# Kernel tuning notes

Hardware: AMD Instinct MI355X
Metric: run time of the kernel (lower is better)

Reference implementation:

```python
import jax, jax.numpy as jnp
import numpy as np

N, E = 50000, 800000
D_IN, D_HID, D_OUT = 128, 64, 32
NEG_SLOPE = 0.2


def _gat_layer(h_in, src, dst, W, a_s, a_d, b):
    # h_in: [N, din], W: [din, dout]
    h = h_in @ W                                   # [N, dout]
    alpha_src = h @ a_s                            # [N]
    alpha_dst = h @ a_d                            # [N]
    e = jax.nn.leaky_relu(alpha_src[src] + alpha_dst[dst], NEG_SLOPE)  # [E']
    # segment softmax over incoming edges of each dst node
    m = jax.ops.segment_max(e, dst, num_segments=N)
    ex = jnp.exp(e - m[dst])
    s = jax.ops.segment_sum(ex, dst, num_segments=N)
    w = ex / s[dst]                                # [E']
    out = jax.ops.segment_sum(h[src] * w[:, None], dst, num_segments=N)
    return out + b


def setup_inputs() -> dict:
    key = jax.random.key(0)
    ks = jax.random.split(key, 16)
    x = jax.random.normal(ks[0], (N, D_IN), dtype=jnp.float32)
    edge_index = jax.random.randint(ks[1], (2, E), 0, N, dtype=jnp.int64)
    dims = [(D_IN, D_HID), (D_HID, D_HID), (D_HID, D_OUT)]
    inp = {"x": x, "edge_index": edge_index}
    for i, (din, dout) in enumerate(dims):
        sc = 1.0 / np.sqrt(din)
        inp[f"W{i}"] = jax.random.normal(ks[2 + 4 * i], (din, dout), dtype=jnp.float32) * sc
        inp[f"as{i}"] = jax.random.normal(ks[3 + 4 * i], (dout,), dtype=jnp.float32) * 0.1
        inp[f"ad{i}"] = jax.random.normal(ks[4 + 4 * i], (dout,), dtype=jnp.float32) * 0.1
        inp[f"b{i}"] = jnp.zeros((dout,), dtype=jnp.float32)
    return inp


def reference(x, edge_index, W0, as0, ad0, b0, W1, as1, ad1, b1, W2, as2, ad2, b2):
    # add self loops (PyG GATConv default)
    loop = jnp.arange(N, dtype=edge_index.dtype)
    src = jnp.concatenate([edge_index[0], loop])
    dst = jnp.concatenate([edge_index[1], loop])
    h = jax.nn.relu(_gat_layer(x, src, dst, W0, as0, ad0, b0))
    h = jax.nn.relu(_gat_layer(h, src, dst, W1, as1, ad1, b1))
    h = jnp.tanh(_gat_layer(h, src, dst, W2, as2, ad2, b2))
    return h
```

## Files before the change

### kernel.cpp

```cpp
#include <hip/hip_runtime.h>
#include <hip/hip_fp16.h>
#include <math.h>

#define N_NODES 50000
#define E_EDGES 800000
#define ETOT    (E_EDGES + N_NODES)

#define BUCK_SHIFT 9
#define BUCK_SZ   (1 << BUCK_SHIFT)
#define NBUCK ((N_NODES + BUCK_SZ - 1) >> BUCK_SHIFT)
#define BS_EPT 16
#define BS_THREADS 256
#define BS_EPB (BS_THREADS * BS_EPT)
#define BS_NBLK ((ETOT + BS_EPB - 1) / BS_EPB)

template<int DIN, int DOUT>
__global__ __launch_bounds__(256)
void gemm_alpha_kernel(const float* __restrict__ X, const float* __restrict__ W,
                       const float* __restrict__ a_s, const float* __restrict__ a_d,
                       __half* __restrict__ H16, float* __restrict__ asrc,
                       float* __restrict__ adst)
{
    constexpr int COLG = DOUT / 4;
    constexpr int ROWG = 256 / COLG;
    constexpr int BM   = ROWG * 4;
    constexpr int K4   = DIN / 4;

    __shared__ float Xl[BM * DIN];
    __shared__ float Wl[DIN * DOUT];

    const int tid = threadIdx.x;
    const int row0b = blockIdx.x * BM;

    constexpr int WV = DIN * DOUT / 4;
    for (int i = tid; i < WV; i += 256)
        ((float4*)Wl)[i] = ((const float4*)W)[i];

    constexpr int XV = BM * K4;
    for (int i = tid; i < XV; i += 256) {
        int r  = i / K4;
        int j  = i % K4;
        int gr = row0b + r;
        float4 v = make_float4(0.f, 0.f, 0.f, 0.f);
        if (gr < N_NODES) v = ((const float4*)X)[gr * K4 + j];
        *(float4*)&Xl[r * DIN + ((j ^ ((r >> 2) & 7)) << 2)] = v;
    }
    __syncthreads();

    const int tx = tid % COLG;
    const int ty = tid / COLG;
    const int r0 = ty * 4;
    const int c0 = tx * 4;
    const int swz = ty & 7;

    float acc[4][4] = {};
    for (int kk = 0; kk < DIN; kk += 4) {
        float a[4][4], w[4][4];
        const int jk = ((kk >> 2) ^ swz) << 2;
#pragma unroll
        for (int i = 0; i < 4; ++i)
            *(float4*)a[i] = *(const float4*)&Xl[(r0 + i) * DIN + jk];
#pragma unroll
        for (int j = 0; j < 4; ++j)
            *(float4*)w[j] = *(const float4*)&Wl[(kk + j) * DOUT + c0];
#pragma unroll
        for (int i = 0; i < 4; ++i)
#pragma unroll
            for (int j = 0; j < 4; ++j)
                acc[i][j] = fmaf(a[i][0], w[0][j],
                            fmaf(a[i][1], w[1][j],
                            fmaf(a[i][2], w[2][j],
                            fmaf(a[i][3], w[3][j], acc[i][j]))));
    }

    float as4[4], ad4[4];
    *(float4*)as4 = *(const float4*)&a_s[c0];
    *(float4*)ad4 = *(const float4*)&a_d[c0];

#pragma unroll
    for (int i = 0; i < 4; ++i) {
        const int gr = row0b + r0 + i;
        float ps = acc[i][0] * as4[0] + acc[i][1] * as4[1] +
                   acc[i][2] * as4[2] + acc[i][3] * as4[3];
        float pd = acc[i][0] * ad4[0] + acc[i][1] * ad4[1] +
                   acc[i][2] * ad4[2] + acc[i][3] * ad4[3];
#pragma unroll
        for (int off = COLG / 2; off >= 1; off >>= 1) {
            ps += __shfl_xor(ps, off, 64);
            pd += __shfl_xor(pd, off, 64);
        }
        if (gr < N_NODES) {
            __half2 p01 = __floats2half2_rn(acc[i][0], acc[i][1]);
            __half2 p23 = __floats2half2_rn(acc[i][2], acc[i][3]);
            uint2 pk;
            pk.x = *(unsigned int*)&p01;
            pk.y = *(unsigned int*)&p23;
            *(uint2*)&H16[gr * DOUT + c0] = pk;
            if (tx == 0) { asrc[gr] = ps; adst[gr] = pd; }
        }
    }
}

__global__ __launch_bounds__(128)
void zero98_kernel(int* __restrict__ bcnt)
{
    int i = threadIdx.x;
    if (i < NBUCK) bcnt[i] = 0;
}

__global__ __launch_bounds__(BS_THREADS)
void hist_kernel(const int* __restrict__ ei, int* __restrict__ bcnt)
{
    __shared__ int lcnt[NBUCK];
    const int t = threadIdx.x;
    for (int i = t; i < NBUCK; i += BS_THREADS) lcnt[i] = 0;
    __syncthreads();
    const int e0 = blockIdx.x * BS_EPB;
#pragma unroll
    for (int k = 0; k < BS_EPT; ++k) {
        const int eid = e0 + k * BS_THREADS + t;
        if (eid < ETOT) {
            int dst = (eid < E_EDGES) ? ei[E_EDGES + eid] : (eid - E_EDGES);
            atomicAdd(&lcnt[dst >> BUCK_SHIFT], 1);
        }
    }
    __syncthreads();
    for (int i = t; i < NBUCK; i += BS_THREADS)
        if (lcnt[i] > 0) atomicAdd(&bcnt[i], lcnt[i]);
}

__global__ __launch_bounds__(128)
void scan98_kernel(const int* __restrict__ bcnt, int* __restrict__ cur,
                   int* __restrict__ cur0)
{
    __shared__ int lds[128];
    const int t = threadIdx.x;
    const int v = (t < NBUCK) ? bcnt[t] : 0;
    lds[t] = v;
    __syncthreads();
    for (int off = 1; off < 128; off <<= 1) {
        int u = (t >= off) ? lds[t - off] : 0;
        __syncthreads();
        lds[t] += u;
        __syncthreads();
    }
    if (t < NBUCK) { cur[t] = lds[t] - v; cur0[t] = lds[t] - v; }
}

__global__ __launch_bounds__(BS_THREADS)
void binscatter_kernel(const int* __restrict__ ei, int* __restrict__ cur,
                       unsigned int* __restrict__ tmp)
{
    __shared__ int lcnt[NBUCK];
    __shared__ int lbase[NBUCK];
    const int t = threadIdx.x;
    for (int i = t; i < NBUCK; i += BS_THREADS) lcnt[i] = 0;
    __syncthreads();

    const int e0 = blockIdx.x * BS_EPB;
    unsigned int pk[BS_EPT];
    int rk[BS_EPT];
    int bk[BS_EPT];
#pragma unroll
    for (int k = 0; k < BS_EPT; ++k) {
        const int eid = e0 + k * BS_THREADS + t;
        bk[k] = -1;
        if (eid < ETOT) {
            int src, dst;
            if (eid < E_EDGES) { src = ei[eid]; dst = ei[E_EDGES + eid]; }
            else               { src = dst = eid - E_EDGES; }
            bk[k] = dst >> BUCK_SHIFT;
            pk[k] = ((unsigned int)dst << 16) | (unsigned int)src;
            rk[k] = atomicAdd(&lcnt[bk[k]], 1);
        }
    }
    __syncthreads();
    for (int i = t; i < NBUCK; i += BS_THREADS)
        if (lcnt[i] > 0) lbase[i] = atomicAdd(&cur[i], lcnt[i]);
    __syncthreads();
#pragma unroll
    for (int k = 0; k < BS_EPT; ++k)
        if (bk[k] >= 0) tmp[lbase[bk[k]] + rk[k]] = pk[k];
}

__global__ __launch_bounds__(BUCK_SZ)
void bucket_sort_kernel(const unsigned int* __restrict__ tmp,
                        const int* __restrict__ cur0,
                        const int* __restrict__ bcnt,
                        unsigned int* __restrict__ csr_pk,
                        int* __restrict__ offs)
{
    __shared__ int lcnt[BUCK_SZ];
    __shared__ int loff[BUCK_SZ];
    __shared__ int lcur[BUCK_SZ];
    const int bk = blockIdx.x;
    const int t  = threadIdx.x;
    const int base = cur0[bk];
    const int cnt  = bcnt[bk];

    lcnt[t] = 0;
    __syncthreads();
    for (int i = t; i < cnt; i += BUCK_SZ)
        atomicAdd(&lcnt[(tmp[base + i] >> 16) & (BUCK_SZ - 1)], 1);
    __syncthreads();

    const int v = lcnt[t];
    loff[t] = v;
    __syncthreads();
    for (int off = 1; off < BUCK_SZ; off <<= 1) {
        int u = (t >= off) ? loff[t - off] : 0;
        __syncthreads();
        loff[t] += u;
        __syncthreads();
    }
    const int excl = loff[t] - v;

    const int g = (bk << BUCK_SHIFT) + t;
    if (g <= N_NODES) offs[g] = base + excl;

    lcur[t] = excl;
    __syncthreads();
    for (int i = t; i < cnt; i += BUCK_SZ) {
        const unsigned int pk = tmp[base + i];
        const int l = (pk >> 16) & (BUCK_SZ - 1);
        const int pos = atomicAdd(&lcur[l], 1);
        csr_pk[base + pos] = pk;
    }
}

__global__ __launch_bounds__(256)
void edge_score_kernel(const unsigned int* __restrict__ csr_pk,
                       const float* __restrict__ asrc,
                       const float* __restrict__ adst,
                       float* __restrict__ pbuf)
{
    int i = blockIdx.x * blockDim.x + threadIdx.x;
    if (i >= ETOT) return;
    const unsigned int pk = csr_pk[i];
    float v = asrc[pk & 0xffffu] + adst[pk >> 16];
    v = (v > 0.f) ? v : 0.2f * v;
    pbuf[i] = __expf(fminf(v, 80.f));
}

template<int DOUT, int ACT>
__global__ __launch_bounds__(256)
void node_agg_kernel(const int* __restrict__ offs,
                     const unsigned int* __restrict__ csr_pk,
                     const float* __restrict__ pbuf,
                     const __half* __restrict__ H16,
                     const float* __restrict__ b,
                     float* __restrict__ out)
{
    constexpr int FL    = DOUT / 4;
    constexpr int SLOTS = 64 / FL;
    const int wv   = threadIdx.x >> 6;
    const int lane = threadIdx.x & 63;
    const int fl   = lane % FL;
    const int slot = lane / FL;
    const int node = blockIdx.x * 4 + wv;
    if (node >= N_NODES) return;

    const int beg = offs[node];
    const int end = offs[node + 1];
    const __half* __restrict__ Hf = H16 + fl * 4;

    float s = 0.f;
    float4 acc = make_float4(0.f, 0.f, 0.f, 0.f);

    for (int cb = beg; cb < end; cb += SLOTS) {
        const int eid = cb + slot;
        float p = 0.f;
        uint2 h8 = make_uint2(0u, 0u);
        if (eid < end) {
            const unsigned int pk = csr_pk[eid];
            p  = pbuf[eid];
            h8 = *(const uint2*)(Hf + (pk & 0xffffu) * DOUT);
        }
        const float2 f01 = __half22float2(*(const __half2*)&h8.x);
        const float2 f23 = __half22float2(*(const __half2*)&h8.y);
        s += p;
        acc.x = fmaf(p, f01.x, acc.x);
        acc.y = fmaf(p, f01.y, acc.y);
        acc.z = fmaf(p, f23.x, acc.z);
        acc.w = fmaf(p, f23.y, acc.w);
    }

#pragma unroll
    for (int off = FL; off < 64; off <<= 1) {
        s     += __shfl_xor(s, off, 64);
        acc.x += __shfl_xor(acc.x, off, 64);
        acc.y += __shfl_xor(acc.y, off, 64);
        acc.z += __shfl_xor(acc.z, off, 64);
        acc.w += __shfl_xor(acc.w, off, 64);
    }

    if (slot == 0) {
        const float4 bb = *(const float4*)&b[fl * 4];
        const float inv = 1.f / s;
        float4 v;
        v.x = acc.x * inv + bb.x;
        v.y = acc.y * inv + bb.y;
        v.z = acc.z * inv + bb.z;
        v.w = acc.w * inv + bb.w;
        if (ACT == 0) {
            v.x = fmaxf(v.x, 0.f); v.y = fmaxf(v.y, 0.f);
            v.z = fmaxf(v.z, 0.f); v.w = fmaxf(v.w, 0.f);
        } else {
            v.x = tanhf(v.x); v.y = tanhf(v.y);
            v.z = tanhf(v.z); v.w = tanhf(v.w);
        }
        *(float4*)&out[node * DOUT + fl * 4] = v;
    }
}


template<int DIN, int DOUT, int ACT>
static void run_layer(const float* X, const float* W, const float* a_s,
                      const float* a_d, const float* b,
                      const int* offs, const unsigned int* csr_pk,
                      float* pbuf, __half* H16, float* asrc, float* adst,
                      float* out, hipStream_t stream)
{
    constexpr int COLG = DOUT / 4;
    constexpr int BM = (256 / COLG) * 4;
    const int gemm_grid = (N_NODES + BM - 1) / BM;
    gemm_alpha_kernel<DIN, DOUT><<<gemm_grid, 256, 0, stream>>>(
        X, W, a_s, a_d, H16, asrc, adst);

    const int egrid = (ETOT + 255) / 256;
    edge_score_kernel<<<egrid, 256, 0, stream>>>(csr_pk, asrc, adst, pbuf);

    const int agg_grid = (N_NODES + 3) / 4;
    node_agg_kernel<DOUT, ACT><<<agg_grid, 256, 0, stream>>>(
        offs, csr_pk, pbuf, H16, b, out);
}

extern "C" void kernel_launch(void* const* d_in, const int* in_sizes, int n_in,
                              void* d_out, int out_size, void* d_ws, size_t ws_size,
                              hipStream_t stream)
{
    const float* x  = (const float*)d_in[0];
    const int*   ei = (const int*)d_in[1];
    const float* W0 = (const float*)d_in[2];
    const float* as0= (const float*)d_in[3];
    const float* ad0= (const float*)d_in[4];
    const float* b0 = (const float*)d_in[5];
    const float* W1 = (const float*)d_in[6];
    const float* as1= (const float*)d_in[7];
    const float* ad1= (const float*)d_in[8];
    const float* b1 = (const float*)d_in[9];
    const float* W2 = (const float*)d_in[10];
    const float* as2= (const float*)d_in[11];
    const float* ad2= (const float*)d_in[12];
    const float* b2 = (const float*)d_in[13];
    float* out = (float*)d_out;

    char* wsb = (char*)d_ws;
    auto take = [&](size_t bytes) {
        char* p = wsb;
        wsb += (bytes + 255) & ~size_t(255);
        return p;
    };
    __half* h16    = (__half*)take(sizeof(__half) * N_NODES * 64);
    float* buf_act = (float*)take(sizeof(float) * N_NODES * 64);
    float* pbuf    = (float*)take(sizeof(float) * ETOT);
    float* asrc    = (float*)take(sizeof(float) * N_NODES);
    float* adst    = (float*)take(sizeof(float) * N_NODES);
    int*   offs    = (int*)take(sizeof(int) * (N_NODES + 1));
    int*   bcnt    = (int*)take(sizeof(int) * NBUCK);
    int*   cur     = (int*)take(sizeof(int) * NBUCK);
    int*   cur0    = (int*)take(sizeof(int) * NBUCK);
    unsigned int* csr_pk = (unsigned int*)take(sizeof(unsigned int) * ETOT);
    unsigned int* tmp = (unsigned int*)h16;

    const int egrid = (ETOT + 255) / 256;
    zero98_kernel<<<1, 128, 0, stream>>>(bcnt);
    hist_kernel<<<BS_NBLK, BS_THREADS, 0, stream>>>(ei, bcnt);
    scan98_kernel<<<1, 128, 0, stream>>>(bcnt, cur, cur0);
    binscatter_kernel<<<BS_NBLK, BS_THREADS, 0, stream>>>(ei, cur, tmp);
    bucket_sort_kernel<<<NBUCK, BUCK_SZ, 0, stream>>>(tmp, cur0, bcnt,
                                                      csr_pk, offs);

    run_layer<128, 64, 0>(x, W0, as0, ad0, b0, offs, csr_pk, pbuf,
                          h16, asrc, adst, buf_act, stream);
    run_layer<64, 64, 0>(buf_act, W1, as1, ad1, b1, offs, csr_pk, pbuf,
                         h16, asrc, adst, buf_act, stream);
    run_layer<64, 32, 1>(buf_act, W2, as2, ad2, b2, offs, csr_pk, pbuf,
                         h16, asrc, adst, out, stream);
}
```

Before: 203.9 us.

## Fuse CSR build into cooperative kernel and inline edge scores into aggregation

Replaces the five CSR-construction launches with a single cooperative kernel that uses grid-wide syncs between the histogram, scan, bin-scatter and bucket-sort phases. The separate edge_score kernel and its pbuf buffer are removed; the aggregation kernel now computes the leaky-relu exponent per edge inline from asrc and the node's adst. Aggregation also moves to 8 features per lane with 16-byte half loads and prefetches the next packed edge. The aim is fewer launches and less edge-sized global traffic. The cost is that the cooperative launch needs all blocks co-resident, and recomputing the exponent inside the gather loop adds work there.

```diff
diff --git a/kernel.cpp b/kernel.cpp
--- a/kernel.cpp
+++ b/kernel.cpp
@@ -1,6 +1,9 @@
 #include <hip/hip_runtime.h>
 #include <hip/hip_fp16.h>
+#include <hip/hip_cooperative_groups.h>
 #include <math.h>
+
+namespace cg = cooperative_groups;
 
 #define N_NODES 50000
 #define E_EDGES 800000
@@ -9,10 +12,10 @@
 #define BUCK_SHIFT 9
 #define BUCK_SZ   (1 << BUCK_SHIFT)
 #define NBUCK ((N_NODES + BUCK_SZ - 1) >> BUCK_SHIFT)
-#define BS_EPT 16
-#define BS_THREADS 256
-#define BS_EPB (BS_THREADS * BS_EPT)
-#define BS_NBLK ((ETOT + BS_EPB - 1) / BS_EPB)
+#define CSR_THREADS 512
+#define CSR_EPT 8
+#define CSR_EPB (CSR_THREADS * CSR_EPT)
+#define CSR_NBLK ((ETOT + CSR_EPB - 1) / CSR_EPB)
 
 template<int DIN, int DOUT>
 __global__ __launch_bounds__(256)
@@ -101,157 +104,126 @@
     }
 }
 
-__global__ __launch_bounds__(128)
-void zero98_kernel(int* __restrict__ bcnt)
-{
-    int i = threadIdx.x;
-    if (i < NBUCK) bcnt[i] = 0;
-}
-
-__global__ __launch_bounds__(BS_THREADS)
-void hist_kernel(const int* __restrict__ ei, int* __restrict__ bcnt)
-{
-    __shared__ int lcnt[NBUCK];
-    const int t = threadIdx.x;
-    for (int i = t; i < NBUCK; i += BS_THREADS) lcnt[i] = 0;
+__global__ __launch_bounds__(CSR_THREADS)
+void csr_build_kernel(const int* __restrict__ ei, int* __restrict__ bpart,
+                      int* __restrict__ cur, int* __restrict__ cur0,
+                      int* __restrict__ bcnt, unsigned int* __restrict__ tmp,
+                      unsigned int* __restrict__ csr_pk, int* __restrict__ offs)
+{
+    cg::grid_group grid = cg::this_grid();
+    __shared__ int lcnt[CSR_THREADS];
+    __shared__ int lextra[CSR_THREADS];
+    const int t   = threadIdx.x;
+    const int blk = blockIdx.x;
+
+    if (t < NBUCK) lcnt[t] = 0;
     __syncthreads();
-    const int e0 = blockIdx.x * BS_EPB;
-#pragma unroll
-    for (int k = 0; k < BS_EPT; ++k) {
-        const int eid = e0 + k * BS_THREADS + t;
-        if (eid < ETOT) {
-            int dst = (eid < E_EDGES) ? ei[E_EDGES + eid] : (eid - E_EDGES);
-            atomicAdd(&lcnt[dst >> BUCK_SHIFT], 1);
+    {
+        const int e0 = blk * CSR_EPB;
+#pragma unroll
+        for (int k = 0; k < CSR_EPT; ++k) {
+            const int eid = e0 + k * CSR_THREADS + t;
+            if (eid < ETOT) {
+                int dst = (eid < E_EDGES) ? ei[E_EDGES + eid] : (eid - E_EDGES);
+                atomicAdd(&lcnt[dst >> BUCK_SHIFT], 1);
+            }
         }
     }
     __syncthreads();
-    for (int i = t; i < NBUCK; i += BS_THREADS)
-        if (lcnt[i] > 0) atomicAdd(&bcnt[i], lcnt[i]);
-}
-
-__global__ __launch_bounds__(128)
-void scan98_kernel(const int* __restrict__ bcnt, int* __restrict__ cur,
-                   int* __restrict__ cur0)
-{
-    __shared__ int lds[128];
-    const int t = threadIdx.x;
-    const int v = (t < NBUCK) ? bcnt[t] : 0;
-    lds[t] = v;
-    __syncthreads();
-    for (int off = 1; off < 128; off <<= 1) {
-        int u = (t >= off) ? lds[t - off] : 0;
-        __syncthreads();
-        lds[t] += u;
-        __syncthreads();
-    }
-    if (t < NBUCK) { cur[t] = lds[t] - v; cur0[t] = lds[t] - v; }
-}
-
-__global__ __launch_bounds__(BS_THREADS)
-void binscatter_kernel(const int* __restrict__ ei, int* __restrict__ cur,
-                       unsigned int* __restrict__ tmp)
-{
-    __shared__ int lcnt[NBUCK];
-    __shared__ int lbase[NBUCK];
-    const int t = threadIdx.x;
-    for (int i = t; i < NBUCK; i += BS_THREADS) lcnt[i] = 0;
-    __syncthreads();
-
-    const int e0 = blockIdx.x * BS_EPB;
-    unsigned int pk[BS_EPT];
-    int rk[BS_EPT];
-    int bk[BS_EPT];
-#pragma unroll
-    for (int k = 0; k < BS_EPT; ++k) {
-        const int eid = e0 + k * BS_THREADS + t;
-        bk[k] = -1;
-        if (eid < ETOT) {
-            int src, dst;
-            if (eid < E_EDGES) { src = ei[eid]; dst = ei[E_EDGES + eid]; }
-            else               { src = dst = eid - E_EDGES; }
-            bk[k] = dst >> BUCK_SHIFT;
-            pk[k] = ((unsigned int)dst << 16) | (unsigned int)src;
-            rk[k] = atomicAdd(&lcnt[bk[k]], 1);
-        }
-    }
-    __syncthreads();
-    for (int i = t; i < NBUCK; i += BS_THREADS)
-        if (lcnt[i] > 0) lbase[i] = atomicAdd(&cur[i], lcnt[i]);
-    __syncthreads();
-#pragma unroll
-    for (int k = 0; k < BS_EPT; ++k)
-        if (bk[k] >= 0) tmp[lbase[bk[k]] + rk[k]] = pk[k];
-}
-
-__global__ __launch_bounds__(BUCK_SZ)
-void bucket_sort_kernel(const unsigned int* __restrict__ tmp,
-                        const int* __restrict__ cur0,
-                        const int* __restrict__ bcnt,
-                        unsigned int* __restrict__ csr_pk,
-                        int* __restrict__ offs)
-{
-    __shared__ int lcnt[BUCK_SZ];
-    __shared__ int loff[BUCK_SZ];
-    __shared__ int lcur[BUCK_SZ];
-    const int bk = blockIdx.x;
-    const int t  = threadIdx.x;
-    const int base = cur0[bk];
-    const int cnt  = bcnt[bk];
-
-    lcnt[t] = 0;
-    __syncthreads();
-    for (int i = t; i < cnt; i += BUCK_SZ)
-        atomicAdd(&lcnt[(tmp[base + i] >> 16) & (BUCK_SZ - 1)], 1);
-    __syncthreads();
-
-    const int v = lcnt[t];
-    loff[t] = v;
-    __syncthreads();
-    for (int off = 1; off < BUCK_SZ; off <<= 1) {
-        int u = (t >= off) ? loff[t - off] : 0;
-        __syncthreads();
-        loff[t] += u;
-        __syncthreads();
-    }
-    const int excl = loff[t] - v;
-
-    const int g = (bk << BUCK_SHIFT) + t;
-    if (g <= N_NODES) offs[g] = base + excl;
-
-    lcur[t] = excl;
-    __syncthreads();
-    for (int i = t; i < cnt; i += BUCK_SZ) {
-        const unsigned int pk = tmp[base + i];
-        const int l = (pk >> 16) & (BUCK_SZ - 1);
-        const int pos = atomicAdd(&lcur[l], 1);
-        csr_pk[base + pos] = pk;
-    }
-}
-
-__global__ __launch_bounds__(256)
-void edge_score_kernel(const unsigned int* __restrict__ csr_pk,
-                       const float* __restrict__ asrc,
-                       const float* __restrict__ adst,
-                       float* __restrict__ pbuf)
-{
-    int i = blockIdx.x * blockDim.x + threadIdx.x;
-    if (i >= ETOT) return;
-    const unsigned int pk = csr_pk[i];
-    float v = asrc[pk & 0xffffu] + adst[pk >> 16];
-    v = (v > 0.f) ? v : 0.2f * v;
-    pbuf[i] = __expf(fminf(v, 80.f));
+    if (t < NBUCK) bpart[t * CSR_NBLK + blk] = lcnt[t];
+    grid.sync();
+
+    if (blk == 0) {
+        int v = 0;
+        if (t < NBUCK) {
+            const int* row = bpart + t * CSR_NBLK;
+            for (int i = 0; i < CSR_NBLK; ++i) v += row[i];
+        }
+        lcnt[t] = (t < NBUCK) ? v : 0;
+        __syncthreads();
+        for (int off = 1; off < 128; off <<= 1) {
+            int u = (t >= off && t < 128) ? lcnt[t - off] : 0;
+            __syncthreads();
+            if (t < 128) lcnt[t] += u;
+            __syncthreads();
+        }
+        if (t < NBUCK) {
+            const int base = lcnt[t] - v;
+            cur[t] = base; cur0[t] = base; bcnt[t] = v;
+        }
+    }
+    grid.sync();
+
+    {
+        if (t < NBUCK) lcnt[t] = 0;
+        __syncthreads();
+        const int e0 = blk * CSR_EPB;
+        unsigned int pk[CSR_EPT];
+        int rk[CSR_EPT];
+        int bk[CSR_EPT];
+#pragma unroll
+        for (int k = 0; k < CSR_EPT; ++k) {
+            const int eid = e0 + k * CSR_THREADS + t;
+            bk[k] = -1;
+            if (eid < ETOT) {
+                int src, dst;
+                if (eid < E_EDGES) { src = ei[eid]; dst = ei[E_EDGES + eid]; }
+                else               { src = dst = eid - E_EDGES; }
+                bk[k] = dst >> BUCK_SHIFT;
+                pk[k] = ((unsigned int)dst << 16) | (unsigned int)src;
+                rk[k] = atomicAdd(&lcnt[bk[k]], 1);
+            }
+        }
+        __syncthreads();
+        if (t < NBUCK && lcnt[t] > 0) lextra[t] = atomicAdd(&cur[t], lcnt[t]);
+        __syncthreads();
+#pragma unroll
+        for (int k = 0; k < CSR_EPT; ++k)
+            if (bk[k] >= 0) tmp[lextra[bk[k]] + rk[k]] = pk[k];
+    }
+    grid.sync();
+
+    if (blk < NBUCK) {
+        const int base = cur0[blk];
+        const int cnt  = bcnt[blk];
+        lcnt[t] = 0;
+        __syncthreads();
+        for (int i = t; i < cnt; i += CSR_THREADS)
+            atomicAdd(&lcnt[(tmp[base + i] >> 16) & (BUCK_SZ - 1)], 1);
+        __syncthreads();
+        const int v = lcnt[t];
+        lextra[t] = v;
+        __syncthreads();
+        for (int off = 1; off < BUCK_SZ; off <<= 1) {
+            int u = (t >= off) ? lextra[t - off] : 0;
+            __syncthreads();
+            lextra[t] += u;
+            __syncthreads();
+        }
+        const int excl = lextra[t] - v;
+        const int g = (blk << BUCK_SHIFT) + t;
+        if (g <= N_NODES) offs[g] = base + excl;
+        lcnt[t] = excl;
+        __syncthreads();
+        for (int i = t; i < cnt; i += CSR_THREADS) {
+            const unsigned int pk = tmp[base + i];
+            const int pos = atomicAdd(&lcnt[(pk >> 16) & (BUCK_SZ - 1)], 1);
+            csr_pk[base + pos] = pk;
+        }
+    }
 }
 
 template<int DOUT, int ACT>
 __global__ __launch_bounds__(256)
 void node_agg_kernel(const int* __restrict__ offs,
                      const unsigned int* __restrict__ csr_pk,
-                     const float* __restrict__ pbuf,
+                     const float* __restrict__ asrc,
+                     const float* __restrict__ adst,
                      const __half* __restrict__ H16,
                      const float* __restrict__ b,
                      float* __restrict__ out)
 {
-    constexpr int FL    = DOUT / 4;
+    constexpr int FL    = DOUT / 8;
     constexpr int SLOTS = 64 / FL;
     const int wv   = threadIdx.x >> 6;
     const int lane = threadIdx.x & 63;
@@ -262,54 +234,65 @@
 
     const int beg = offs[node];
     const int end = offs[node + 1];
-    const __half* __restrict__ Hf = H16 + fl * 4;
+    const float adn = adst[node];
+    const __half* __restrict__ Hf = H16 + fl * 8;
 
     float s = 0.f;
-    float4 acc = make_float4(0.f, 0.f, 0.f, 0.f);
+    float acc[8] = {};
+
+    int eid = beg + slot;
+    bool valid = (eid < end);
+    unsigned int pk = valid ? csr_pk[eid] : 0u;
 
     for (int cb = beg; cb < end; cb += SLOTS) {
-        const int eid = cb + slot;
+        const int nid = cb + SLOTS + slot;
+        const bool nvalid = (nid < end);
+        const unsigned int npk = nvalid ? csr_pk[nid] : 0u;
+
         float p = 0.f;
-        uint2 h8 = make_uint2(0u, 0u);
-        if (eid < end) {
-            const unsigned int pk = csr_pk[eid];
-            p  = pbuf[eid];
-            h8 = *(const uint2*)(Hf + (pk & 0xffffu) * DOUT);
-        }
-        const float2 f01 = __half22float2(*(const __half2*)&h8.x);
-        const float2 f23 = __half22float2(*(const __half2*)&h8.y);
+        uint4 h = make_uint4(0u, 0u, 0u, 0u);
+        if (valid) {
+            const unsigned int src = pk & 0xffffu;
+            float v = asrc[src] + adn;
+            v = fmaxf(v, 0.2f * v);
+            p = __expf(fminf(v, 80.f));
+            h = *(const uint4*)(Hf + src * DOUT);
+        }
+        const float2 f0 = __half22float2(*(const __half2*)&h.x);
+        const float2 f1 = __half22float2(*(const __half2*)&h.y);
+        const float2 f2 = __half22float2(*(const __half2*)&h.z);
+        const float2 f3 = __half22float2(*(const __half2*)&h.w);
         s += p;
-        acc.x = fmaf(p, f01.x, acc.x);
-        acc.y = fmaf(p, f01.y, acc.y);
-        acc.z = fmaf(p, f23.x, acc.z);
-        acc.w = fmaf(p, f23.y, acc.w);
+        acc[0] = fmaf(p, f0.x, acc[0]);
+        acc[1] = fmaf(p, f0.y, acc[1]);
+        acc[2] = fmaf(p, f1.x, acc[2]);
+        acc[3] = fmaf(p, f1.y, acc[3]);
+        acc[4] = fmaf(p, f2.x, acc[4]);
+        acc[5] = fmaf(p, f2.y, acc[5]);
+        acc[6] = fmaf(p, f3.x, acc[6]);
+        acc[7] = fmaf(p, f3.y, acc[7]);
+        valid = nvalid;
+        pk = npk;
     }
 
 #pragma unroll
     for (int off = FL; off < 64; off <<= 1) {
-        s     += __shfl_xor(s, off, 64);
-        acc.x += __shfl_xor(acc.x, off, 64);
-        acc.y += __shfl_xor(acc.y, off, 64);
-        acc.z += __shfl_xor(acc.z, off, 64);
-        acc.w += __shfl_xor(acc.w, off, 64);
+        s += __shfl_xor(s, off, 64);
+#pragma unroll
+        for (int j = 0; j < 8; ++j)
+            acc[j] += __shfl_xor(acc[j], off, 64);
     }
 
     if (slot == 0) {
-        const float4 bb = *(const float4*)&b[fl * 4];
         const float inv = 1.f / s;
-        float4 v;
-        v.x = acc.x * inv + bb.x;
-        v.y = acc.y * inv + bb.y;
-        v.z = acc.z * inv + bb.z;
-        v.w = acc.w * inv + bb.w;
-        if (ACT == 0) {
-            v.x = fmaxf(v.x, 0.f); v.y = fmaxf(v.y, 0.f);
-            v.z = fmaxf(v.z, 0.f); v.w = fmaxf(v.w, 0.f);
-        } else {
-            v.x = tanhf(v.x); v.y = tanhf(v.y);
-            v.z = tanhf(v.z); v.w = tanhf(v.w);
-        }
-        *(float4*)&out[node * DOUT + fl * 4] = v;
+        float o[8];
+#pragma unroll
+        for (int j = 0; j < 8; ++j) {
+            float v = acc[j] * inv + b[fl * 8 + j];
+            o[j] = (ACT == 0) ? fmaxf(v, 0.f) : tanhf(v);
+        }
+        *(float4*)&out[node * DOUT + fl * 8]     = *(float4*)&o[0];
+        *(float4*)&out[node * DOUT + fl * 8 + 4] = *(float4*)&o[4];
     }
 }
 
@@ -318,7 +301,7 @@
 static void run_layer(const float* X, const float* W, const float* a_s,
                       const float* a_d, const float* b,
                       const int* offs, const unsigned int* csr_pk,
-                      float* pbuf, __half* H16, float* asrc, float* adst,
+                      __half* H16, float* asrc, float* adst,
                       float* out, hipStream_t stream)
 {
     constexpr int COLG = DOUT / 4;
@@ -327,12 +310,9 @@
     gemm_alpha_kernel<DIN, DOUT><<<gemm_grid, 256, 0, stream>>>(
         X, W, a_s, a_d, H16, asrc, adst);
 
-    const int egrid = (ETOT + 255) / 256;
-    edge_score_kernel<<<egrid, 256, 0, stream>>>(csr_pk, asrc, adst, pbuf);
-
     const int agg_grid = (N_NODES + 3) / 4;
     node_agg_kernel<DOUT, ACT><<<agg_grid, 256, 0, stream>>>(
-        offs, csr_pk, pbuf, H16, b, out);
+        offs, csr_pk, asrc, adst, H16, b, out);
 }
 
 extern "C" void kernel_launch(void* const* d_in, const int* in_sizes, int n_in,
@@ -363,28 +343,28 @@
     };
     __half* h16    = (__half*)take(sizeof(__half) * N_NODES * 64);
     float* buf_act = (float*)take(sizeof(float) * N_NODES * 64);
-    float* pbuf    = (float*)take(sizeof(float) * ETOT);
     float* asrc    = (float*)take(sizeof(float) * N_NODES);
     float* adst    = (float*)take(sizeof(float) * N_NODES);
     int*   offs    = (int*)take(sizeof(int) * (N_NODES + 1));
     int*   bcnt    = (int*)take(sizeof(int) * NBUCK);
     int*   cur     = (int*)take(sizeof(int) * NBUCK);
     int*   cur0    = (int*)take(sizeof(int) * NBUCK);
+    int*   bpart   = (int*)take(sizeof(int) * NBUCK * CSR_NBLK);
     unsigned int* csr_pk = (unsigned int*)take(sizeof(unsigned int) * ETOT);
     unsigned int* tmp = (unsigned int*)h16;
 
-    const int egrid = (ETOT + 255) / 256;
-    zero98_kernel<<<1, 128, 0, stream>>>(bcnt);
-    hist_kernel<<<BS_NBLK, BS_THREADS, 0, stream>>>(ei, bcnt);
-    scan98_kernel<<<1, 128, 0, stream>>>(bcnt, cur, cur0);
-    binscatter_kernel<<<BS_NBLK, BS_THREADS, 0, stream>>>(ei, cur, tmp);
-    bucket_sort_kernel<<<NBUCK, BUCK_SZ, 0, stream>>>(tmp, cur0, bcnt,
-                                                      csr_pk, offs);
-
-    run_layer<128, 64, 0>(x, W0, as0, ad0, b0, offs, csr_pk, pbuf,
+    {
+        void* args[] = { (void*)&ei, (void*)&bpart, (void*)&cur, (void*)&cur0,
+                         (void*)&bcnt, (void*)&tmp, (void*)&csr_pk, (void*)&offs };
+        hipLaunchCooperativeKernel((const void*)csr_build_kernel,
+                                   dim3(CSR_NBLK), dim3(CSR_THREADS),
+                                   args, 0, stream);
+    }
+
+    run_layer<128, 64, 0>(x, W0, as0, ad0, b0, offs, csr_pk,
                           h16, asrc, adst, buf_act, stream);
-    run_layer<64, 64, 0>(buf_act, W1, as1, ad1, b1, offs, csr_pk, pbuf,
+    run_layer<64, 64, 0>(buf_act, W1, as1, ad1, b1, offs, csr_pk,
                          h16, asrc, adst, buf_act, stream);
-    run_layer<64, 32, 1>(buf_act, W2, as2, ad2, b2, offs, csr_pk, pbuf,
+    run_layer<64, 32, 1>(buf_act, W2, as2, ad2, b2, offs, csr_pk,
                          h16, asrc, adst, out, stream);
 }
```

Measured after the change: 256.9 us. +26.0%, slower.
